# Kernel tuning notes

Hardware: AMD Instinct MI355X
Metric: run time of the kernel (lower is better)

The kernel has to match this reference:

```python
import jax, jax.numpy as jnp
import numpy as np

N_NODES = 50000
N_EDGES = 800000
IN_DIM = 128
HID = 128
N_GRAPHS = 256


def setup_inputs() -> dict:
    key = jax.random.key(0)
    ks = jax.random.split(key, 12)
    x = jax.random.normal(ks[0], (N_NODES, IN_DIM), dtype=jnp.float32)
    edge_index = jax.random.randint(ks[1], (2, N_EDGES), 0, N_NODES, dtype=jnp.int64)
    batch = jnp.sort(jax.random.randint(ks[2], (N_NODES,), 0, N_GRAPHS, dtype=jnp.int64))
    s = 1.0 / np.sqrt(IN_DIM)
    sh = 1.0 / np.sqrt(HID)
    params = {
        # GraphConv layer 1: out = aggr_add(x_j) @ W_rel + b_rel + x @ W_root
        "w1_rel": jax.random.uniform(ks[3], (IN_DIM, HID), jnp.float32, -s, s),
        "b1_rel": jax.random.uniform(ks[4], (HID,), jnp.float32, -s, s),
        "w1_root": jax.random.uniform(ks[5], (IN_DIM, HID), jnp.float32, -s, s),
        "w2_rel": jax.random.uniform(ks[6], (HID, HID), jnp.float32, -sh, sh),
        "b2_rel": jax.random.uniform(ks[7], (HID,), jnp.float32, -sh, sh),
        "w2_root": jax.random.uniform(ks[8], (HID, HID), jnp.float32, -sh, sh),
        "fc1_w": jax.random.uniform(ks[9], (HID, HID), jnp.float32, -sh, sh),
        "fc1_b": jnp.zeros((HID,), jnp.float32),
        "fc2_w": jax.random.uniform(ks[10], (HID, 1), jnp.float32, -sh, sh),
        "fc2_b": jnp.zeros((1,), jnp.float32),
    }
    return {"x": x, "edge_index": edge_index, "batch": batch, **params}


def _graph_conv(x, src, dst, w_rel, b_rel, w_root):
    # sum-aggregate neighbor features (gather from src, scatter-add to dst)
    agg = jax.ops.segment_sum(x[src], dst, num_segments=N_NODES)
    return agg @ w_rel + b_rel + x @ w_root


def reference(x, edge_index, batch, w1_rel, b1_rel, w1_root,
              w2_rel, b2_rel, w2_root, fc1_w, fc1_b, fc2_w, fc2_b):
    src, dst = edge_index[0], edge_index[1]
    h = jax.nn.relu(_graph_conv(x, src, dst, w1_rel, b1_rel, w1_root))
    h = jax.nn.relu(_graph_conv(h, src, dst, w2_rel, b2_rel, w2_root))
    # global mean pool over graphs in the batch
    sums = jax.ops.segment_sum(h, batch, num_segments=N_GRAPHS)
    counts = jax.ops.segment_sum(jnp.ones((N_NODES,), h.dtype), batch, num_segments=N_GRAPHS)
    pooled = sums / jnp.maximum(counts, 1.0)[:, None]  # [G, HID]
    out = jax.nn.relu(pooled @ fc1_w + fc1_b)
    return out @ fc2_w + fc2_b  # [G, 1]
```

## Files before the change

kernel.cpp:

```cpp
#include <hip/hip_runtime.h>

#define NNODES 50000
#define NEDGES 800000
#define DIM 128
#define NGRAPHS 256
#define NPAD 50176
#define SCAN_BLOCKS 196

typedef _Float16 half4_t __attribute__((ext_vector_type(4)));
typedef _Float16 half8_t __attribute__((ext_vector_type(8)));
typedef float f32x4 __attribute__((ext_vector_type(4)));

__global__ void cast_x_kernel(const float* __restrict__ x, _Float16* __restrict__ xh) {
    int t = blockIdx.x * 256 + threadIdx.x;
    const float4* x4 = reinterpret_cast<const float4*>(x);
    float4 a = x4[t * 2];
    float4 b = x4[t * 2 + 1];
    half8_t h;
    h[0] = (_Float16)a.x; h[1] = (_Float16)a.y; h[2] = (_Float16)a.z; h[3] = (_Float16)a.w;
    h[4] = (_Float16)b.x; h[5] = (_Float16)b.y; h[6] = (_Float16)b.z; h[7] = (_Float16)b.w;
    *reinterpret_cast<half8_t*>(&xh[(size_t)t * 8]) = h;
}

__global__ void cast_w_kernel(const float* __restrict__ w1_rel, const float* __restrict__ w1_root,
                              const float* __restrict__ w2_rel, const float* __restrict__ w2_root,
                              _Float16* __restrict__ WT1, _Float16* __restrict__ WT2) {
    int t = blockIdx.x * 256 + threadIdx.x;
    int layer = t >> 15;
    int r = t & 32767;
    int c = r >> 8;
    int k = r & 255;
    const float* wr = layer ? w2_rel : w1_rel;
    const float* wo = layer ? w2_root : w1_root;
    float v = (k < 128) ? wr[k * DIM + c] : wo[(k - 128) * DIM + c];
    _Float16* dstp = layer ? WT2 : WT1;
    dstp[(size_t)c * 256 + k] = (_Float16)v;
}

__global__ void hist_kernel(const int* __restrict__ dst, int* __restrict__ deg) {
    int e = blockIdx.x * 256 + threadIdx.x;
    if (e < NEDGES) atomicAdd(&deg[dst[e]], 1);
}

__global__ void scan1_kernel(const int* __restrict__ deg, int* __restrict__ bsum) {
    __shared__ int s[256];
    int t = threadIdx.x;
    s[t] = deg[blockIdx.x * 256 + t];
    __syncthreads();
    #pragma unroll
    for (int d = 128; d > 0; d >>= 1) {
        if (t < d) s[t] += s[t + d];
        __syncthreads();
    }
    if (t == 0) bsum[blockIdx.x] = s[0];
}

__global__ void scan2_kernel(int* __restrict__ bsum) {
    __shared__ int s[256];
    int t = threadIdx.x;
    int v = (t < SCAN_BLOCKS) ? bsum[t] : 0;
    s[t] = v;
    __syncthreads();
    #pragma unroll
    for (int d = 1; d < 256; d <<= 1) {
        int u = (t >= d) ? s[t - d] : 0;
        __syncthreads();
        s[t] += u;
        __syncthreads();
    }
    if (t < SCAN_BLOCKS) bsum[t] = (t == 0) ? 0 : s[t - 1];
}

__global__ void scan3_kernel(const int* __restrict__ deg,
                             const int* __restrict__ bsum,
                             int* __restrict__ offs,
                             int* __restrict__ curs) {
    __shared__ int s[256];
    int t = threadIdx.x;
    int idx = blockIdx.x * 256 + t;
    s[t] = deg[idx];
    __syncthreads();
    #pragma unroll
    for (int d = 1; d < 256; d <<= 1) {
        int u = (t >= d) ? s[t - d] : 0;
        __syncthreads();
        s[t] += u;
        __syncthreads();
    }
    int excl = ((t == 0) ? 0 : s[t - 1]) + bsum[blockIdx.x];
    if (idx <= NNODES) {
        offs[idx] = excl;
        curs[idx] = excl;
    }
}

__global__ void bucket_kernel(const int* __restrict__ src,
                              const int* __restrict__ dst,
                              int* __restrict__ curs,
                              int* __restrict__ srcs_sorted) {
    int e = blockIdx.x * 256 + threadIdx.x;
    if (e >= NEDGES) return;
    int pos = atomicAdd(&curs[dst[e]], 1);
    __builtin_nontemporal_store(src[e], &srcs_sorted[pos]);
}

__global__ void gather_agg_kernel(const _Float16* __restrict__ feat,
                                  const int* __restrict__ offs,
                                  const int* __restrict__ srcs_sorted,
                                  _Float16* __restrict__ agg) {
    int n = blockIdx.x * 16 + (threadIdx.x >> 4);
    int q = threadIdx.x & 15;
    if (n >= NNODES) return;
    int beg = offs[n], end = offs[n + 1];
    float a0[8] = {0.f, 0.f, 0.f, 0.f, 0.f, 0.f, 0.f, 0.f};
    float a1[8] = {0.f, 0.f, 0.f, 0.f, 0.f, 0.f, 0.f, 0.f};
    int i = beg;
    for (; i + 4 <= end; i += 4) {
        int s0 = srcs_sorted[i + 0];
        int s1 = srcs_sorted[i + 1];
        int s2 = srcs_sorted[i + 2];
        int s3 = srcs_sorted[i + 3];
        half8_t v0 = *reinterpret_cast<const half8_t*>(&feat[(size_t)s0 * DIM + q * 8]);
        half8_t v1 = *reinterpret_cast<const half8_t*>(&feat[(size_t)s1 * DIM + q * 8]);
        half8_t v2 = *reinterpret_cast<const half8_t*>(&feat[(size_t)s2 * DIM + q * 8]);
        half8_t v3 = *reinterpret_cast<const half8_t*>(&feat[(size_t)s3 * DIM + q * 8]);
        #pragma unroll
        for (int j = 0; j < 8; ++j) {
            a0[j] += (float)v0[j] + (float)v1[j];
            a1[j] += (float)v2[j] + (float)v3[j];
        }
    }
    for (; i < end; ++i) {
        half8_t v = *reinterpret_cast<const half8_t*>(&feat[(size_t)srcs_sorted[i] * DIM + q * 8]);
        #pragma unroll
        for (int j = 0; j < 8; ++j) a0[j] += (float)v[j];
    }
    half8_t r;
    #pragma unroll
    for (int j = 0; j < 8; ++j) r[j] = (_Float16)(a0[j] + a1[j]);
    *reinterpret_cast<half8_t*>(&agg[(size_t)n * DIM + q * 8]) = r;
}

__global__ __launch_bounds__(256) void conv_mfma_kernel(
        const _Float16* __restrict__ Ah,
        const _Float16* Xh,
        const _Float16* __restrict__ WT,
        const float* __restrict__ bias,
        _Float16* outh) {
    const int wave = threadIdx.x >> 6;
    const int lane = threadIdx.x & 63;
    const int row0 = blockIdx.x * 128 + wave * 32;
    const int rA = lane & 15;
    const int kg = lane >> 4;

    f32x4 acc[2][8];
    #pragma unroll
    for (int m = 0; m < 2; ++m)
        #pragma unroll
        for (int nt = 0; nt < 8; ++nt)
            acc[m][nt] = (f32x4){0.f, 0.f, 0.f, 0.f};

    int ra0 = row0 + rA;        if (ra0 > NNODES - 1) ra0 = NNODES - 1;
    int ra1 = row0 + 16 + rA;   if (ra1 > NNODES - 1) ra1 = NNODES - 1;

    #pragma unroll
    for (int ks = 0; ks < 8; ++ks) {
        const _Float16* srcb = (ks < 4) ? Ah : Xh;
        const int klocal = (ks & 3) * 32 + kg * 8;
        half8_t a0 = *reinterpret_cast<const half8_t*>(&srcb[(size_t)ra0 * DIM + klocal]);
        half8_t a1 = *reinterpret_cast<const half8_t*>(&srcb[(size_t)ra1 * DIM + klocal]);
        const int kglob = ks * 32 + kg * 8;
        #pragma unroll
        for (int nt = 0; nt < 8; ++nt) {
            half8_t b = *reinterpret_cast<const half8_t*>(&WT[(size_t)(nt * 16 + rA) * 256 + kglob]);
            acc[0][nt] = __builtin_amdgcn_mfma_f32_16x16x32_f16(a0, b, acc[0][nt], 0, 0, 0);
            acc[1][nt] = __builtin_amdgcn_mfma_f32_16x16x32_f16(a1, b, acc[1][nt], 0, 0, 0);
        }
    }

    const int ccol = lane & 15;
    const int crow4 = (lane >> 4) * 4;
    #pragma unroll
    for (int m = 0; m < 2; ++m) {
        #pragma unroll
        for (int nt = 0; nt < 8; ++nt) {
            float bb = bias[nt * 16 + ccol];
            #pragma unroll
            for (int r = 0; r < 4; ++r) {
                int row = row0 + m * 16 + crow4 + r;
                if (row < NNODES) {
                    float v = acc[m][nt][r] + bb;
                    outh[(size_t)row * DIM + nt * 16 + ccol] = (_Float16)(v > 0.f ? v : 0.f);
                }
            }
        }
    }
}

__global__ void pool_mlp_kernel(const _Float16* __restrict__ h,
                                const int* __restrict__ batch,
                                const float* __restrict__ fc1_w,
                                const float* __restrict__ fc1_b,
                                const float* __restrict__ fc2_w,
                                const float* __restrict__ fc2_b,
                                float* __restrict__ out) {
    __shared__ float p[DIM];
    __shared__ float red[DIM];
    int g = blockIdx.x;
    int c = threadIdx.x;
    int lo = 0, hi = NNODES;
    while (lo < hi) { int m = (lo + hi) >> 1; if (batch[m] < g) lo = m + 1; else hi = m; }
    int beg = lo;
    hi = NNODES;
    while (lo < hi) { int m = (lo + hi) >> 1; if (batch[m] < g + 1) lo = m + 1; else hi = m; }
    int end = lo;
    float acc0 = 0.f, acc1 = 0.f;
    int n = beg;
    for (; n + 2 <= end; n += 2) {
        acc0 += (float)h[(size_t)n * DIM + c];
        acc1 += (float)h[(size_t)(n + 1) * DIM + c];
    }
    if (n < end) acc0 += (float)h[(size_t)n * DIM + c];
    float cnt = (float)(end - beg);
    p[c] = (acc0 + acc1) / fmaxf(cnt, 1.f);
    __syncthreads();
    float acc = fc1_b[c];
    for (int k = 0; k < DIM; ++k) acc = fmaf(p[k], fc1_w[k * DIM + c], acc);
    acc = acc > 0.f ? acc : 0.f;
    red[c] = acc * fc2_w[c];
    __syncthreads();
    #pragma unroll
    for (int s = 64; s > 0; s >>= 1) {
        if (c < s) red[c] += red[c + s];
        __syncthreads();
    }
    if (c == 0) out[g] = red[0] + fc2_b[0];
}

extern "C" void kernel_launch(void* const* d_in, const int* in_sizes, int n_in,
                              void* d_out, int out_size, void* d_ws, size_t ws_size,
                              hipStream_t stream) {
    const float* x       = (const float*)d_in[0];
    const int*   ei      = (const int*)d_in[1];
    const int*   batch   = (const int*)d_in[2];
    const float* w1_rel  = (const float*)d_in[3];
    const float* b1_rel  = (const float*)d_in[4];
    const float* w1_root = (const float*)d_in[5];
    const float* w2_rel  = (const float*)d_in[6];
    const float* b2_rel  = (const float*)d_in[7];
    const float* w2_root = (const float*)d_in[8];
    const float* fc1_w   = (const float*)d_in[9];
    const float* fc1_b   = (const float*)d_in[10];
    const float* fc2_w   = (const float*)d_in[11];
    const float* fc2_b   = (const float*)d_in[12];
    float* out = (float*)d_out;

    char* ws = (char*)d_ws;
    const size_t feath_bytes = (size_t)NNODES * DIM * sizeof(_Float16);
    _Float16* Ah  = (_Float16*)ws;
    _Float16* Hh  = (_Float16*)(ws + feath_bytes);
    _Float16* xh  = (_Float16*)(ws + 2 * feath_bytes);
    _Float16* WT1 = (_Float16*)(ws + 3 * feath_bytes);
    _Float16* WT2 = WT1 + 128 * 256;
    int*   deg    = (int*)(WT2 + 128 * 256);
    int*   offs   = deg + NPAD;
    int*   curs   = offs + NPAD;
    int*   bsum   = curs + NPAD;
    int*   srcs   = bsum + 256;

    const int* src = ei;
    const int* dst = ei + NEDGES;

    const int edge_blocks = (NEDGES + 255) / 256;
    const int conv_blocks = (NNODES + 127) / 128;
    const int agg_blocks  = (NNODES + 15) / 16;

    cast_x_kernel<<<(NNODES * DIM / 8) / 256, 256, 0, stream>>>(x, xh);
    cast_w_kernel<<<256, 256, 0, stream>>>(w1_rel, w1_root, w2_rel, w2_root, WT1, WT2);

    hipMemsetAsync(deg, 0, NPAD * sizeof(int), stream);
    hist_kernel<<<edge_blocks, 256, 0, stream>>>(dst, deg);
    scan1_kernel<<<SCAN_BLOCKS, 256, 0, stream>>>(deg, bsum);
    scan2_kernel<<<1, 256, 0, stream>>>(bsum);
    scan3_kernel<<<SCAN_BLOCKS, 256, 0, stream>>>(deg, bsum, offs, curs);
    bucket_kernel<<<edge_blocks, 256, 0, stream>>>(src, dst, curs, srcs);

    gather_agg_kernel<<<agg_blocks, 256, 0, stream>>>(xh, offs, srcs, Ah);
    conv_mfma_kernel<<<conv_blocks, 256, 0, stream>>>(Ah, xh, WT1, b1_rel, Hh);

    gather_agg_kernel<<<agg_blocks, 256, 0, stream>>>(Hh, offs, srcs, Ah);
    conv_mfma_kernel<<<conv_blocks, 256, 0, stream>>>(Ah, Hh, WT2, b2_rel, Hh);

    pool_mlp_kernel<<<NGRAPHS, 128, 0, stream>>>(Hh, batch, fc1_w, fc1_b, fc2_w, fc2_b, out);
}
```

Before: 346.7 us.

## Partition edge atomics by XCD and fuse cast/hist into one prep kernel

Merges the x cast, weight transpose-cast and degree histogram into a single prep kernel, which saves launches. The histogram and bucket kernels now assign each block a destination-node range keyed to blockIdx mod 8, so that atomics on a given counter come from blocks likely placed on the same XCD and stay local to its L2. The cost is that each edge chunk's dst values are read eight times, once per XCD group. The bucket store also drops its nontemporal hint.

```diff
diff --git a/kernel.cpp b/kernel.cpp
--- a/kernel.cpp
+++ b/kernel.cpp
@@ -6,40 +6,55 @@
 #define NGRAPHS 256
 #define NPAD 50176
 #define SCAN_BLOCKS 196
-
-typedef _Float16 half4_t __attribute__((ext_vector_type(4)));
+#define NXCD 8
+#define NODES_PER_XCD (NNODES / NXCD)
+#define GB 391
+#define EPB 2048
+
 typedef _Float16 half8_t __attribute__((ext_vector_type(8)));
 typedef float f32x4 __attribute__((ext_vector_type(4)));
 
-__global__ void cast_x_kernel(const float* __restrict__ x, _Float16* __restrict__ xh) {
-    int t = blockIdx.x * 256 + threadIdx.x;
-    const float4* x4 = reinterpret_cast<const float4*>(x);
-    float4 a = x4[t * 2];
-    float4 b = x4[t * 2 + 1];
-    half8_t h;
-    h[0] = (_Float16)a.x; h[1] = (_Float16)a.y; h[2] = (_Float16)a.z; h[3] = (_Float16)a.w;
-    h[4] = (_Float16)b.x; h[5] = (_Float16)b.y; h[6] = (_Float16)b.z; h[7] = (_Float16)b.w;
-    *reinterpret_cast<half8_t*>(&xh[(size_t)t * 8]) = h;
-}
-
-__global__ void cast_w_kernel(const float* __restrict__ w1_rel, const float* __restrict__ w1_root,
-                              const float* __restrict__ w2_rel, const float* __restrict__ w2_root,
-                              _Float16* __restrict__ WT1, _Float16* __restrict__ WT2) {
-    int t = blockIdx.x * 256 + threadIdx.x;
-    int layer = t >> 15;
-    int r = t & 32767;
-    int c = r >> 8;
-    int k = r & 255;
-    const float* wr = layer ? w2_rel : w1_rel;
-    const float* wo = layer ? w2_root : w1_root;
-    float v = (k < 128) ? wr[k * DIM + c] : wo[(k - 128) * DIM + c];
-    _Float16* dstp = layer ? WT2 : WT1;
-    dstp[(size_t)c * 256 + k] = (_Float16)v;
-}
-
-__global__ void hist_kernel(const int* __restrict__ dst, int* __restrict__ deg) {
-    int e = blockIdx.x * 256 + threadIdx.x;
-    if (e < NEDGES) atomicAdd(&deg[dst[e]], 1);
+__global__ void prep_kernel(const float* __restrict__ x, _Float16* __restrict__ xh,
+                            const float* __restrict__ w1_rel, const float* __restrict__ w1_root,
+                            const float* __restrict__ w2_rel, const float* __restrict__ w2_root,
+                            _Float16* __restrict__ WT1, _Float16* __restrict__ WT2,
+                            const int* __restrict__ dst, int* __restrict__ deg) {
+    int tid = blockIdx.x * 256 + threadIdx.x;
+
+    if (tid < (NNODES * DIM / 8)) {
+        const float4* x4 = reinterpret_cast<const float4*>(x);
+        float4 a = x4[tid * 2];
+        float4 b = x4[tid * 2 + 1];
+        half8_t h;
+        h[0] = (_Float16)a.x; h[1] = (_Float16)a.y; h[2] = (_Float16)a.z; h[3] = (_Float16)a.w;
+        h[4] = (_Float16)b.x; h[5] = (_Float16)b.y; h[6] = (_Float16)b.z; h[7] = (_Float16)b.w;
+        *reinterpret_cast<half8_t*>(&xh[(size_t)tid * 8]) = h;
+    }
+
+    if (tid < 2 * DIM * 256) {
+        int layer = tid >> 15;
+        int r = tid & 32767;
+        int c = r >> 8;
+        int k = r & 255;
+        const float* wr = layer ? w2_rel : w1_rel;
+        const float* wo = layer ? w2_root : w1_root;
+        float v = (k < 128) ? wr[k * DIM + c] : wo[(k - 128) * DIM + c];
+        _Float16* dstp = layer ? WT2 : WT1;
+        dstp[(size_t)c * 256 + k] = (_Float16)v;
+    }
+
+    int g  = blockIdx.x & (NXCD - 1);
+    int bb = blockIdx.x >> 3;
+    int lo = g * NODES_PER_XCD, hi = lo + NODES_PER_XCD;
+    int base = bb * EPB + threadIdx.x;
+    #pragma unroll
+    for (int i = 0; i < 8; ++i) {
+        int e = base + i * 256;
+        if (e < NEDGES) {
+            int d = dst[e];
+            if (d >= lo && d < hi) atomicAdd(&deg[d], 1);
+        }
+    }
 }
 
 __global__ void scan1_kernel(const int* __restrict__ deg, int* __restrict__ bsum) {
@@ -98,10 +113,21 @@
                               const int* __restrict__ dst,
                               int* __restrict__ curs,
                               int* __restrict__ srcs_sorted) {
-    int e = blockIdx.x * 256 + threadIdx.x;
-    if (e >= NEDGES) return;
-    int pos = atomicAdd(&curs[dst[e]], 1);
-    __builtin_nontemporal_store(src[e], &srcs_sorted[pos]);
+    int g  = blockIdx.x & (NXCD - 1);
+    int bb = blockIdx.x >> 3;
+    int lo = g * NODES_PER_XCD, hi = lo + NODES_PER_XCD;
+    int base = bb * EPB + threadIdx.x;
+    #pragma unroll
+    for (int i = 0; i < 8; ++i) {
+        int e = base + i * 256;
+        if (e < NEDGES) {
+            int d = dst[e];
+            if (d >= lo && d < hi) {
+                int pos = atomicAdd(&curs[d], 1);
+                srcs_sorted[pos] = src[e];
+            }
+        }
+    }
 }
 
 __global__ void gather_agg_kernel(const _Float16* __restrict__ feat,
@@ -271,19 +297,18 @@
     const int* src = ei;
     const int* dst = ei + NEDGES;
 
-    const int edge_blocks = (NEDGES + 255) / 256;
+    const int xcd_blocks  = GB * NXCD;
     const int conv_blocks = (NNODES + 127) / 128;
     const int agg_blocks  = (NNODES + 15) / 16;
 
-    cast_x_kernel<<<(NNODES * DIM / 8) / 256, 256, 0, stream>>>(x, xh);
-    cast_w_kernel<<<256, 256, 0, stream>>>(w1_rel, w1_root, w2_rel, w2_root, WT1, WT2);
-
     hipMemsetAsync(deg, 0, NPAD * sizeof(int), stream);
-    hist_kernel<<<edge_blocks, 256, 0, stream>>>(dst, deg);
+    prep_kernel<<<xcd_blocks, 256, 0, stream>>>(x, xh, w1_rel, w1_root, w2_rel, w2_root,
+                                                WT1, WT2, dst, deg);
+
     scan1_kernel<<<SCAN_BLOCKS, 256, 0, stream>>>(deg, bsum);
     scan2_kernel<<<1, 256, 0, stream>>>(bsum);
     scan3_kernel<<<SCAN_BLOCKS, 256, 0, stream>>>(deg, bsum, offs, curs);
-    bucket_kernel<<<edge_blocks, 256, 0, stream>>>(src, dst, curs, srcs);
+    bucket_kernel<<<xcd_blocks, 256, 0, stream>>>(src, dst, curs, srcs);
 
     gather_agg_kernel<<<agg_blocks, 256, 0, stream>>>(xh, offs, srcs, Ah);
     conv_mfma_kernel<<<conv_blocks, 256, 0, stream>>>(Ah, xh, WT1, b1_rel, Hh);
```

New measurement: 324.3 us. 1.07x faster.
